# Optimization experiments

Hardware: AMD Instinct MI355X
Metric: run time of the kernel (lower is better)

## Reference

```python
import jax, jax.numpy as jnp
import numpy as np

N = 25600          # total nodes
B = 64             # graphs in batch
NPG = N // B       # nodes per graph (400)
K = 16             # in-degree (regular graph)
E = N * K          # edges
D = 128            # hidden dim = out dim
L = 4              # DGN layers
NUM_ATOM = 128


def _linear_init(key, out_s, in_s):
    lim = 1.0 / np.sqrt(in_s)
    return jax.random.uniform(key, (out_s, in_s), jnp.float32, -lim, lim)


def setup_inputs() -> dict:
    key = jax.random.key(0)
    ks = jax.random.split(key, 16)
    node_feat = jax.random.randint(ks[0], (N,), 0, NUM_ATOM)
    # K-regular in-degree graph, edges intra-graph; dst sorted
    dst = jnp.repeat(jnp.arange(N), K)                       # [E]
    src_local = jax.random.randint(ks[1], (E,), 0, NPG)
    src = (dst // NPG) * NPG + src_local                     # same graph as dst
    eig = jax.random.normal(ks[2], (E, 2), jnp.float32)
    snorm_n = jnp.full((N, 1), 1.0 / np.sqrt(NPG), jnp.float32)
    graph_ids = jnp.arange(N) // NPG
    emb = jax.random.normal(ks[3], (NUM_ATOM, D), jnp.float32) * 0.02
    pre_W = jnp.stack([_linear_init(jax.random.fold_in(ks[4], i), D, 2 * D) for i in range(L)])
    pre_b = jnp.zeros((L, D), jnp.float32)
    post_W = jnp.stack([_linear_init(jax.random.fold_in(ks[5], i), D, 5 * D) for i in range(L)])
    post_b = jnp.zeros((L, D), jnp.float32)
    r_W0 = _linear_init(ks[6], 64, 128); r_b0 = jnp.zeros((64,), jnp.float32)
    r_W1 = _linear_init(ks[7], 32, 64);  r_b1 = jnp.zeros((32,), jnp.float32)
    r_W2 = _linear_init(ks[8], 128, 32); r_b2 = jnp.zeros((128,), jnp.float32)
    return dict(node_feat=node_feat, src=src, dst=dst, eig=eig, snorm_n=snorm_n,
                graph_ids=graph_ids, emb=emb, pre_W=pre_W, pre_b=pre_b,
                post_W=post_W, post_b=post_b, r_W0=r_W0, r_b0=r_b0,
                r_W1=r_W1, r_b1=r_b1, r_W2=r_W2, r_b2=r_b2)


def _dgn_layer(h, src, dst, eig, snorm_n, Wp, bp, Wq, bq):
    n = h.shape[0]
    # pretrans on edges: Linear(cat(h_src, h_dst))  [E, D]
    z2 = jnp.concatenate([h[src], h[dst]], axis=-1)
    e = jnp.einsum('ei,oi->eo', z2, Wp) + bp
    seg_sum = lambda v: jax.ops.segment_sum(v, dst, num_segments=n, indices_are_sorted=True)
    s = seg_sum(e)
    mean = s / K
    mx = jax.ops.segment_max(e, dst, num_segments=n, indices_are_sorted=True)
    # directional aggregator (eig_idx=1)
    w = eig[:, 1]
    denom = seg_sum(jnp.abs(w)) + 1e-8                       # [n]
    ew = w / denom[dst]                                      # [E]
    dir_agg = jnp.abs(seg_sum(e * ew[:, None]) - seg_sum(ew)[:, None] * h)
    agg = jnp.concatenate([h, mean, s, mx, dir_agg], axis=-1)  # [n, 5D]
    hn = jnp.einsum('ni,oi->no', agg, Wq) + bq
    hn = hn * snorm_n           # graph_norm
    hn = jax.nn.relu(hn)
    return h + hn               # residual (in_dim == out_dim)


def reference(node_feat, src, dst, eig, snorm_n, graph_ids, emb,
              pre_W, pre_b, post_W, post_b,
              r_W0, r_b0, r_W1, r_b1, r_W2, r_b2):
    h = emb[node_feat]                                       # AtomEncoder
    for i in range(L):
        h = _dgn_layer(h, src, dst, eig, snorm_n, pre_W[i], pre_b[i], post_W[i], post_b[i])
    # mean_nodes per graph (equal-sized graphs)
    hg = jax.ops.segment_sum(h, graph_ids, num_segments=B, indices_are_sorted=True) / NPG
    y = jax.nn.relu(hg @ r_W0.T + r_b0)
    y = jax.nn.relu(y @ r_W1.T + r_b1)
    return y @ r_W2.T + r_b2                                 # [B, 128]
```

## Files before the change

kernel.cpp:

```cpp
#include <hip/hip_runtime.h>
#include <cstddef>

#define NN 25600
#define BB 64
#define NPG 400
#define KK 16
#define LL 4

typedef _Float16 half_t;
typedef _Float16 h8 __attribute__((ext_vector_type(8)));
typedef _Float16 h4 __attribute__((ext_vector_type(4)));
typedef _Float16 h2 __attribute__((ext_vector_type(2)));
typedef float f32x4 __attribute__((ext_vector_type(4)));

__global__ __launch_bounds__(256) void prep_k(const float* __restrict__ preW,
                                              const float* __restrict__ preb,
                                              const float* __restrict__ postW,
                                              half_t* __restrict__ WpreH,
                                              half_t* __restrict__ WpreL,
                                              float* __restrict__ bpre,
                                              half_t* __restrict__ WpostH,
                                              half_t* __restrict__ WpostL) {
  int idx = blockIdx.x * 256 + threadIdx.x;
  const int n1 = LL * 256 * 128;
  const int n2 = n1 + LL * 256;
  const int n3 = n2 + LL * 128 * 512;
  if (idx < n1) {
    int l = idx / 32768;
    int q = idx % 32768;
    int j = q & 7, lane = (q >> 3) & 63, kc = (q >> 9) & 3, c16 = q >> 11;
    int col = c16 * 16 + (lane & 15);
    int k = kc * 32 + (lane >> 4) * 8 + j;
    float v = (col < 128) ? preW[(size_t)l * 32768 + (size_t)col * 256 + k]
                          : preW[(size_t)l * 32768 + (size_t)(col - 128) * 256 + 128 + k];
    half_t hi = (half_t)v;
    WpreH[idx] = hi;
    WpreL[idx] = (half_t)(v - (float)hi);
  } else if (idx < n2) {
    int r = idx - n1;
    int l = r / 256, o = r % 256;
    bpre[r] = (o < 128) ? 0.f : preb[l * 128 + (o - 128)];
  } else if (idx < n3) {
    int r = idx - n2;
    int l = r / 65536;
    int q = r % 65536;
    int j = q & 7, lane = (q >> 3) & 63, kc = (q >> 9) & 15, c16 = q >> 13;
    int col = c16 * 16 + (lane & 15);
    int k = kc * 32 + (lane >> 4) * 8 + j;
    int jblk = k >> 7, kk = k & 127;
    const float* base = postW + (size_t)l * 128 * 640 + (size_t)col * 640;
    float v;
    if (jblk == 0)      v = base[kk];
    else if (jblk == 1) v = base[128 + kk] * (1.f / 16.f) + base[256 + kk];
    else if (jblk == 2) v = base[384 + kk];
    else                v = base[512 + kk];
    half_t hi = (half_t)v;
    WpostH[r] = hi;
    WpostL[r] = (half_t)(v - (float)hi);
  }
}

__global__ __launch_bounds__(256) void embed_k(const int* __restrict__ nf,
                                               const float* __restrict__ emb,
                                               half_t* __restrict__ Hh,
                                               half_t* __restrict__ Hl) {
  int idx = blockIdx.x * 256 + threadIdx.x;
  int n = idx >> 5;
  int d4 = idx & 31;
  int a = nf[n];
  float4 v = *(const float4*)(emb + (size_t)a * 128 + d4 * 4);
  h4 hi, lo;
  const float* vp = &v.x;
#pragma unroll
  for (int j = 0; j < 4; ++j) {
    half_t h = (half_t)vp[j];
    hi[j] = h;
    lo[j] = (half_t)(vp[j] - (float)h);
  }
  *(h4*)(Hh + (size_t)n * 128 + d4 * 4) = hi;
  *(h4*)(Hl + (size_t)n * 128 + d4 * 4) = lo;
}

__global__ __launch_bounds__(256) void pre_gemm_k(const half_t* __restrict__ Ah_g,
                                                  const half_t* __restrict__ Al_g,
                                                  const half_t* __restrict__ Wh_g,
                                                  const half_t* __restrict__ Wl_g,
                                                  float* __restrict__ preA) {
  __shared__ half_t Ahs[64][132];
  __shared__ half_t Als[64][132];
  const int tid = threadIdx.x;
  const int bid = blockIdx.x;
  const int swz = (bid & 7) * 50 + (bid >> 3);
  const int r0 = swz * 64;
  const int wid = tid >> 6, lane = tid & 63;
  const int wm = wid >> 1, wn = wid & 1;
  const int lr = lane & 15, lk = (lane >> 4) * 8;
  f32x4 acc[2][4] = {};

  {
    const int row = tid >> 2;
#pragma unroll
    for (int s = 0; s < 4; ++s) {
      const int koff = (tid & 3) * 8 + s * 32;
      const size_t g = (size_t)(r0 + row) * 128 + koff;
      *(h8*)&Ahs[row][koff] = *(const h8*)(Ah_g + g);
      *(h8*)&Als[row][koff] = *(const h8*)(Al_g + g);
    }
  }
  __syncthreads();

#pragma unroll
  for (int kc = 0; kc < 4; ++kc) {
    h8 af[2][2];
#pragma unroll
    for (int mi = 0; mi < 2; ++mi) {
      const int r = wm * 32 + mi * 16 + lr;
      af[mi][0] = *(const h8*)&Ahs[r][kc * 32 + lk];
      af[mi][1] = *(const h8*)&Als[r][kc * 32 + lk];
    }
#pragma unroll
    for (int nj = 0; nj < 4; ++nj) {
      const size_t fi = ((size_t)((wn * 4 + nj) * 4 + kc) * 64 + lane) * 8;
      const h8 b0v = *(const h8*)(Wh_g + fi);
      const h8 b1v = *(const h8*)(Wl_g + fi);
#pragma unroll
      for (int mi = 0; mi < 2; ++mi) {
        acc[mi][nj] = __builtin_amdgcn_mfma_f32_16x16x32_f16(af[mi][0], b0v, acc[mi][nj], 0, 0, 0);
        acc[mi][nj] = __builtin_amdgcn_mfma_f32_16x16x32_f16(af[mi][0], b1v, acc[mi][nj], 0, 0, 0);
        acc[mi][nj] = __builtin_amdgcn_mfma_f32_16x16x32_f16(af[mi][1], b0v, acc[mi][nj], 0, 0, 0);
      }
    }
  }
#pragma unroll
  for (int mi = 0; mi < 2; ++mi) {
    const int rowb = r0 + wm * 32 + mi * 16 + (lane >> 4) * 4;
#pragma unroll
    for (int nj = 0; nj < 4; ++nj) {
      const int col = wn * 64 + nj * 16 + lr;
#pragma unroll
      for (int q = 0; q < 4; ++q) {
        preA[(size_t)(rowb + q) * 128 + col] = acc[mi][nj][q];
      }
    }
  }
}

__global__ __launch_bounds__(256, 3) void agg_post_k(const float* __restrict__ preA,
                                                     const int* __restrict__ src,
                                                     const float* __restrict__ eig,
                                                     const half_t* __restrict__ WpHg,
                                                     const half_t* __restrict__ WpLg,
                                                     const float* __restrict__ bpre128,
                                                     half_t* __restrict__ Hh,
                                                     half_t* __restrict__ Hl,
                                                     const half_t* __restrict__ Wh,
                                                     const half_t* __restrict__ Wl,
                                                     const float* __restrict__ bias,
                                                     const float* __restrict__ snorm) {
  __shared__ half_t Ah[16][392];
  __shared__ half_t Al[16][392];
  __shared__ float bsh[16][132];
  const int tid = threadIdx.x;
  const int bid = blockIdx.x;
  const int swz = (bid & 7) * 200 + (bid >> 3);
  const int r0 = swz * 16;
  const int wid = tid >> 6, lane = tid & 63;
  const int wn = wid;
  const int lr = lane & 15, lk = (lane >> 4) * 8;
  const int gsel = lane >> 5;
  const int m4 = (lane & 31) * 4;

  const int frow = r0 + lr;
  h8 afh[4][2];
#pragma unroll
  for (int hc = 0; hc < 4; ++hc) {
    afh[hc][0] = *(const h8*)(Hh + (size_t)frow * 128 + hc * 32 + lk);
    afh[hc][1] = *(const h8*)(Hl + (size_t)frow * 128 + hc * 32 + lk);
  }

  {
    f32x4 bacc[2] = {};
#pragma unroll
    for (int kc = 0; kc < 4; ++kc) {
#pragma unroll
      for (int nj = 0; nj < 2; ++nj) {
        const size_t fi = ((size_t)((8 + wn * 2 + nj) * 4 + kc) * 64 + lane) * 8;
        const h8 b0v = *(const h8*)(WpHg + fi);
        const h8 b1v = *(const h8*)(WpLg + fi);
        bacc[nj] = __builtin_amdgcn_mfma_f32_16x16x32_f16(afh[kc][0], b0v, bacc[nj], 0, 0, 0);
        bacc[nj] = __builtin_amdgcn_mfma_f32_16x16x32_f16(afh[kc][0], b1v, bacc[nj], 0, 0, 0);
        bacc[nj] = __builtin_amdgcn_mfma_f32_16x16x32_f16(afh[kc][1], b0v, bacc[nj], 0, 0, 0);
      }
    }
    const int rowb = (lane >> 4) * 4;
#pragma unroll
    for (int nj = 0; nj < 2; ++nj) {
      const int col = (wn * 2 + nj) * 16 + lr;
      const float bv = bpre128[col];
#pragma unroll
      for (int q = 0; q < 4; ++q) {
        bsh[rowb + q][col] = bacc[nj][q] + bv;
      }
    }
  }
  __syncthreads();

#pragma unroll
  for (int i = 0; i < 4; ++i) {
    const int lrow = wid * 4 + i;
    const int n = r0 + lrow;
    int sv[KK];
    float wv[KK];
    {
      const int4* sp4 = (const int4*)(src + (size_t)n * KK);
      const float4* ep4 = (const float4*)(eig + (size_t)n * KK * 2);
#pragma unroll
      for (int t = 0; t < 4; ++t) {
        const int4 s4 = sp4[t];
        sv[4 * t + 0] = s4.x;
        sv[4 * t + 1] = s4.y;
        sv[4 * t + 2] = s4.z;
        sv[4 * t + 3] = s4.w;
      }
#pragma unroll
      for (int t = 0; t < 8; ++t) {
        const float4 e4 = ep4[t];
        wv[2 * t + 0] = e4.y;
        wv[2 * t + 1] = e4.w;
      }
    }
    float4 g0 = *(const float4*)(preA + (size_t)sv[0 + gsel] * 128 + m4);
    float4 g1 = *(const float4*)(preA + (size_t)sv[2 + gsel] * 128 + m4);
    float4 g2 = *(const float4*)(preA + (size_t)sv[4 + gsel] * 128 + m4);
    float4 g3 = *(const float4*)(preA + (size_t)sv[6 + gsel] * 128 + m4);
    float4 g4 = *(const float4*)(preA + (size_t)sv[8 + gsel] * 128 + m4);
    float4 g5 = *(const float4*)(preA + (size_t)sv[10 + gsel] * 128 + m4);
    float4 g6 = *(const float4*)(preA + (size_t)sv[12 + gsel] * 128 + m4);
    float4 g7 = *(const float4*)(preA + (size_t)sv[14 + gsel] * 128 + m4);
    float denom = 0.f;
#pragma unroll
    for (int e = 0; e < KK; ++e) denom += fabsf(wv[e]);
    denom += 1e-8f;
    const float inv = 1.f / denom;
    float sum_ew = 0.f;
#pragma unroll
    for (int e = 0; e < KK; ++e) {
      wv[e] *= inv;
      sum_ew += wv[e];
    }
    float sx = 0.f, sy = 0.f, sz = 0.f, sw_ = 0.f;
    float wx = 0.f, wy = 0.f, wz = 0.f, ww = 0.f;
    float mx = -3.402823466e+38f, my = mx, mz = mx, mw = mx;
#define ACC(G, J)                                                   \
    {                                                               \
      const float we = wv[2 * (J) + gsel];                          \
      sx += G.x; sy += G.y; sz += G.z; sw_ += G.w;                  \
      wx = fmaf(we, G.x, wx); wy = fmaf(we, G.y, wy);               \
      wz = fmaf(we, G.z, wz); ww = fmaf(we, G.w, ww);               \
      mx = fmaxf(mx, G.x); my = fmaxf(my, G.y);                     \
      mz = fmaxf(mz, G.z); mw = fmaxf(mw, G.w);                     \
    }
    ACC(g0, 0) ACC(g1, 1) ACC(g2, 2) ACC(g3, 3)
    ACC(g4, 4) ACC(g5, 5) ACC(g6, 6) ACC(g7, 7)
#undef ACC
    sx += __shfl_xor(sx, 32); sy += __shfl_xor(sy, 32);
    sz += __shfl_xor(sz, 32); sw_ += __shfl_xor(sw_, 32);
    wx += __shfl_xor(wx, 32); wy += __shfl_xor(wy, 32);
    wz += __shfl_xor(wz, 32); ww += __shfl_xor(ww, 32);
    mx = fmaxf(mx, __shfl_xor(mx, 32)); my = fmaxf(my, __shfl_xor(my, 32));
    mz = fmaxf(mz, __shfl_xor(mz, 32)); mw = fmaxf(mw, __shfl_xor(mw, 32));

    if (lane < 32) {
      const float4 b4 = *(const float4*)&bsh[lrow][m4];
      const h4 hh4 = *(const h4*)(Hh + (size_t)n * 128 + m4);
      const h4 hl4 = *(const h4*)(Hl + (size_t)n * 128 + m4);
      const float h0 = (float)hh4[0] + (float)hl4[0];
      const float h1 = (float)hh4[1] + (float)hl4[1];
      const float h2v = (float)hh4[2] + (float)hl4[2];
      const float h3 = (float)hh4[3] + (float)hl4[3];
      auto wr4 = [&](int kcol, float v0, float v1, float v2, float v3) {
        h4 hi, lo;
        hi[0] = (half_t)v0; lo[0] = (half_t)(v0 - (float)hi[0]);
        hi[1] = (half_t)v1; lo[1] = (half_t)(v1 - (float)hi[1]);
        hi[2] = (half_t)v2; lo[2] = (half_t)(v2 - (float)hi[2]);
        hi[3] = (half_t)v3; lo[3] = (half_t)(v3 - (float)hi[3]);
        *(h4*)&Ah[lrow][kcol] = hi;
        *(h4*)&Al[lrow][kcol] = lo;
      };
      wr4(m4, sx + 16.f * b4.x, sy + 16.f * b4.y, sz + 16.f * b4.z, sw_ + 16.f * b4.w);
      wr4(128 + m4, mx + b4.x, my + b4.y, mz + b4.z, mw + b4.w);
      wr4(256 + m4,
          fabsf(wx + sum_ew * (b4.x - h0)), fabsf(wy + sum_ew * (b4.y - h1)),
          fabsf(wz + sum_ew * (b4.z - h2v)), fabsf(ww + sum_ew * (b4.w - h3)));
    }
  }
  __syncthreads();

  f32x4 acc[2] = {};
#pragma unroll
  for (int kc = 0; kc < 16; ++kc) {
    h8 a0, a1;
    if (kc < 4) {
      a0 = afh[kc & 3][0];
      a1 = afh[kc & 3][1];
    } else {
      a0 = *(const h8*)&Ah[lr][(kc - 4) * 32 + lk];
      a1 = *(const h8*)&Al[lr][(kc - 4) * 32 + lk];
    }
#pragma unroll
    for (int nj = 0; nj < 2; ++nj) {
      const size_t fi = ((size_t)((wn * 2 + nj) * 16 + kc) * 64 + lane) * 8;
      const h8 b0v = *(const h8*)(Wh + fi);
      const h8 b1v = *(const h8*)(Wl + fi);
      acc[nj] = __builtin_amdgcn_mfma_f32_16x16x32_f16(a0, b0v, acc[nj], 0, 0, 0);
      acc[nj] = __builtin_amdgcn_mfma_f32_16x16x32_f16(a0, b1v, acc[nj], 0, 0, 0);
      acc[nj] = __builtin_amdgcn_mfma_f32_16x16x32_f16(a1, b0v, acc[nj], 0, 0, 0);
    }
  }

  const int rowb = r0 + (lane >> 4) * 4;
#pragma unroll
  for (int nj = 0; nj < 2; ++nj) {
    const int col = wn * 32 + nj * 16 + lr;
    const float bv = bias[col];
#pragma unroll
    for (int q = 0; q < 4; ++q) {
      const int r = rowb + q;
      float a = acc[nj][q] + bv;
      a *= snorm[r];
      a = fmaxf(a, 0.f);
      const size_t off = (size_t)r * 128 + col;
      const float hold = (float)Hh[off] + (float)Hl[off];
      const float hn = hold + a;
      const half_t hi = (half_t)hn;
      Hh[off] = hi;
      Hl[off] = (half_t)(hn - (float)hi);
    }
  }
}

__global__ __launch_bounds__(256) void reduce_mlp_k(const half_t* __restrict__ Hh,
                                                    const half_t* __restrict__ Hl,
                                                    const float* __restrict__ W0, const float* __restrict__ b0,
                                                    const float* __restrict__ W1, const float* __restrict__ b1,
                                                    const float* __restrict__ W2, const float* __restrict__ b2,
                                                    float* __restrict__ out) {
  __shared__ float hgs[128];
  __shared__ float red[128];
  __shared__ float y0s[64];
  __shared__ float y1s[32];
  __shared__ float wb[64 * 130];
  const int g = blockIdx.x;
  const int t = threadIdx.x;
  {
    const int d = t & 127, hf = t >> 7;
    const size_t base = ((size_t)g * NPG + (size_t)hf * 200) * 128 + d;
    float acc = 0.f;
    for (int i = 0; i < 200; ++i) {
      const size_t off = base + (size_t)i * 128;
      acc += (float)Hh[off] + (float)Hl[off];
    }
    if (hf) red[d] = acc;
    __syncthreads();
    if (!hf) hgs[d] = (acc + red[d]) * (1.f / (float)NPG);
  }
  __syncthreads();
  for (int idx = t; idx < 64 * 128; idx += 256) {
    wb[(idx >> 7) * 130 + (idx & 127)] = W0[idx];
  }
  __syncthreads();
  if (t < 64) {
    float a = b0[t];
    const float* w = &wb[t * 130];
    for (int k = 0; k < 128; ++k) a = fmaf(hgs[k], w[k], a);
    y0s[t] = fmaxf(a, 0.f);
  }
  __syncthreads();
  for (int idx = t; idx < 32 * 64; idx += 256) {
    wb[(idx >> 6) * 66 + (idx & 63)] = W1[idx];
  }
  __syncthreads();
  if (t < 32) {
    float a = b1[t];
    const float* w = &wb[t * 66];
    for (int k = 0; k < 64; ++k) a = fmaf(y0s[k], w[k], a);
    y1s[t] = fmaxf(a, 0.f);
  }
  __syncthreads();
  for (int idx = t; idx < 128 * 32; idx += 256) {
    wb[(idx >> 5) * 34 + (idx & 31)] = W2[idx];
  }
  __syncthreads();
  if (t < 128) {
    float a = b2[t];
    const float* w = &wb[t * 34];
    for (int k = 0; k < 32; ++k) a = fmaf(y1s[k], w[k], a);
    out[(size_t)g * 128 + t] = a;
  }
}

extern "C" void kernel_launch(void* const* d_in, const int* in_sizes, int n_in,
                              void* d_out, int out_size, void* d_ws, size_t ws_size,
                              hipStream_t stream) {
  const int* node_feat = (const int*)d_in[0];
  const int* src = (const int*)d_in[1];
  const float* eig = (const float*)d_in[3];
  const float* snorm = (const float*)d_in[4];
  const float* emb = (const float*)d_in[6];
  const float* preW = (const float*)d_in[7];
  const float* preb = (const float*)d_in[8];
  const float* postW = (const float*)d_in[9];
  const float* postb = (const float*)d_in[10];
  const float* rW0 = (const float*)d_in[11];
  const float* rb0 = (const float*)d_in[12];
  const float* rW1 = (const float*)d_in[13];
  const float* rb1 = (const float*)d_in[14];
  const float* rW2 = (const float*)d_in[15];
  const float* rb2 = (const float*)d_in[16];
  float* out = (float*)d_out;

  half_t* Hh = (half_t*)d_ws;
  half_t* Hl = Hh + (size_t)NN * 128;
  float* preA = (float*)(Hl + (size_t)NN * 128);
  half_t* WpreH = (half_t*)(preA + (size_t)NN * 128);
  half_t* WpreL = WpreH + (size_t)LL * 32768;
  half_t* WpostH = WpreL + (size_t)LL * 32768;
  half_t* WpostL = WpostH + (size_t)LL * 65536;
  float* bpre = (float*)(WpostL + (size_t)LL * 65536);

  prep_k<<<1540, 256, 0, stream>>>(preW, preb, postW, WpreH, WpreL, bpre, WpostH, WpostL);
  embed_k<<<(NN * 32) / 256, 256, 0, stream>>>(node_feat, emb, Hh, Hl);

  for (int l = 0; l < LL; ++l) {
    pre_gemm_k<<<NN / 64, 256, 0, stream>>>(
        Hh, Hl, WpreH + (size_t)l * 32768, WpreL + (size_t)l * 32768, preA);
    agg_post_k<<<NN / 16, 256, 0, stream>>>(
        preA, src, eig,
        WpreH + (size_t)l * 32768, WpreL + (size_t)l * 32768,
        bpre + (size_t)l * 256 + 128,
        Hh, Hl,
        WpostH + (size_t)l * 65536, WpostL + (size_t)l * 65536,
        postb + (size_t)l * 128, snorm);
  }

  reduce_mlp_k<<<BB, 256, 0, stream>>>(Hh, Hl, rW0, rb0, rW1, rb1, rW2, rb2, out);
}
```

Measured before the change: 267.1 us.

## Split fused aggregate+post-GEMM into separate agg and post-GEMM kernels

The dst-half of the pre-transform GEMM moves into pre_gemm_k as a second grid dimension, which writes a per-node bias buffer. The former fused agg_post_k is split into agg_k, with one wave per node writing the full 512-wide split-fp16 aggregate row to global memory, and post_gemm_k, which loads those rows into LDS and runs the MFMA GEMM. This is meant to raise occupancy and parallelism of the gather phase and remove redundant per-block work. The cost is extra global round trips of the aggregate matrix (hi and lo, 512 halves per node) and one more launch per layer.

```diff
diff --git a/kernel.cpp b/kernel.cpp
--- a/kernel.cpp
+++ b/kernel.cpp
@@ -85,11 +85,14 @@
                                                   const half_t* __restrict__ Al_g,
                                                   const half_t* __restrict__ Wh_g,
                                                   const half_t* __restrict__ Wl_g,
-                                                  float* __restrict__ preA) {
+                                                  const float* __restrict__ bpre128,
+                                                  float* __restrict__ preA,
+                                                  float* __restrict__ bF) {
   __shared__ half_t Ahs[64][132];
   __shared__ half_t Als[64][132];
   const int tid = threadIdx.x;
   const int bid = blockIdx.x;
+  const int y = blockIdx.y;
   const int swz = (bid & 7) * 50 + (bid >> 3);
   const int r0 = swz * 64;
   const int wid = tid >> 6, lane = tid & 63;
@@ -120,7 +123,7 @@
     }
 #pragma unroll
     for (int nj = 0; nj < 4; ++nj) {
-      const size_t fi = ((size_t)((wn * 4 + nj) * 4 + kc) * 64 + lane) * 8;
+      const size_t fi = ((size_t)((y * 8 + wn * 4 + nj) * 4 + kc) * 64 + lane) * 8;
       const h8 b0v = *(const h8*)(Wh_g + fi);
       const h8 b1v = *(const h8*)(Wl_g + fi);
 #pragma unroll
@@ -131,35 +134,134 @@
       }
     }
   }
+  float* outp = (y == 0) ? preA : bF;
 #pragma unroll
   for (int mi = 0; mi < 2; ++mi) {
     const int rowb = r0 + wm * 32 + mi * 16 + (lane >> 4) * 4;
 #pragma unroll
     for (int nj = 0; nj < 4; ++nj) {
       const int col = wn * 64 + nj * 16 + lr;
+      const float bv = (y == 0) ? 0.f : bpre128[col];
 #pragma unroll
       for (int q = 0; q < 4; ++q) {
-        preA[(size_t)(rowb + q) * 128 + col] = acc[mi][nj][q];
+        outp[(size_t)(rowb + q) * 128 + col] = acc[mi][nj][q] + bv;
       }
     }
   }
 }
 
-__global__ __launch_bounds__(256, 3) void agg_post_k(const float* __restrict__ preA,
-                                                     const int* __restrict__ src,
-                                                     const float* __restrict__ eig,
-                                                     const half_t* __restrict__ WpHg,
-                                                     const half_t* __restrict__ WpLg,
-                                                     const float* __restrict__ bpre128,
-                                                     half_t* __restrict__ Hh,
-                                                     half_t* __restrict__ Hl,
-                                                     const half_t* __restrict__ Wh,
-                                                     const half_t* __restrict__ Wl,
-                                                     const float* __restrict__ bias,
-                                                     const float* __restrict__ snorm) {
-  __shared__ half_t Ah[16][392];
-  __shared__ half_t Al[16][392];
-  __shared__ float bsh[16][132];
+__global__ __launch_bounds__(256) void agg_k(const float* __restrict__ preA,
+                                             const float* __restrict__ bF,
+                                             const int* __restrict__ src,
+                                             const float* __restrict__ eig,
+                                             const half_t* __restrict__ Hh,
+                                             const half_t* __restrict__ Hl,
+                                             half_t* __restrict__ AhG,
+                                             half_t* __restrict__ AlG) {
+  const int bid = blockIdx.x;
+  const int swz = (bid & 7) * 800 + (bid >> 3);
+  const int wid = threadIdx.x >> 6, lane = threadIdx.x & 63;
+  const int n = swz * 4 + wid;
+  const int gsel = lane >> 5;
+  const int m4 = (lane & 31) * 4;
+
+  int sv[KK];
+  float wv[KK];
+  {
+    const int4* sp4 = (const int4*)(src + (size_t)n * KK);
+    const float4* ep4 = (const float4*)(eig + (size_t)n * KK * 2);
+#pragma unroll
+    for (int t = 0; t < 4; ++t) {
+      const int4 s4 = sp4[t];
+      sv[4 * t + 0] = s4.x; sv[4 * t + 1] = s4.y;
+      sv[4 * t + 2] = s4.z; sv[4 * t + 3] = s4.w;
+    }
+#pragma unroll
+    for (int t = 0; t < 8; ++t) {
+      const float4 e4 = ep4[t];
+      wv[2 * t + 0] = e4.y; wv[2 * t + 1] = e4.w;
+    }
+  }
+  float4 g0 = *(const float4*)(preA + (size_t)sv[0 + gsel] * 128 + m4);
+  float4 g1 = *(const float4*)(preA + (size_t)sv[2 + gsel] * 128 + m4);
+  float4 g2 = *(const float4*)(preA + (size_t)sv[4 + gsel] * 128 + m4);
+  float4 g3 = *(const float4*)(preA + (size_t)sv[6 + gsel] * 128 + m4);
+  float4 g4 = *(const float4*)(preA + (size_t)sv[8 + gsel] * 128 + m4);
+  float4 g5 = *(const float4*)(preA + (size_t)sv[10 + gsel] * 128 + m4);
+  float4 g6 = *(const float4*)(preA + (size_t)sv[12 + gsel] * 128 + m4);
+  float4 g7 = *(const float4*)(preA + (size_t)sv[14 + gsel] * 128 + m4);
+  float denom = 0.f;
+#pragma unroll
+  for (int e = 0; e < KK; ++e) denom += fabsf(wv[e]);
+  denom += 1e-8f;
+  const float inv = 1.f / denom;
+  float sum_ew = 0.f;
+#pragma unroll
+  for (int e = 0; e < KK; ++e) {
+    wv[e] *= inv;
+    sum_ew += wv[e];
+  }
+  float sx = 0.f, sy = 0.f, sz = 0.f, sw_ = 0.f;
+  float wx = 0.f, wy = 0.f, wz = 0.f, ww = 0.f;
+  float mx = -3.402823466e+38f, my = mx, mz = mx, mw = mx;
+#define ACC(G, J)                                                   \
+  {                                                                 \
+    const float we = wv[2 * (J) + gsel];                            \
+    sx += G.x; sy += G.y; sz += G.z; sw_ += G.w;                    \
+    wx = fmaf(we, G.x, wx); wy = fmaf(we, G.y, wy);                 \
+    wz = fmaf(we, G.z, wz); ww = fmaf(we, G.w, ww);                 \
+    mx = fmaxf(mx, G.x); my = fmaxf(my, G.y);                       \
+    mz = fmaxf(mz, G.z); mw = fmaxf(mw, G.w);                       \
+  }
+  ACC(g0, 0) ACC(g1, 1) ACC(g2, 2) ACC(g3, 3)
+  ACC(g4, 4) ACC(g5, 5) ACC(g6, 6) ACC(g7, 7)
+#undef ACC
+  sx += __shfl_xor(sx, 32); sy += __shfl_xor(sy, 32);
+  sz += __shfl_xor(sz, 32); sw_ += __shfl_xor(sw_, 32);
+  wx += __shfl_xor(wx, 32); wy += __shfl_xor(wy, 32);
+  wz += __shfl_xor(wz, 32); ww += __shfl_xor(ww, 32);
+  mx = fmaxf(mx, __shfl_xor(mx, 32)); my = fmaxf(my, __shfl_xor(my, 32));
+  mz = fmaxf(mz, __shfl_xor(mz, 32)); mw = fmaxf(mw, __shfl_xor(mw, 32));
+
+  if (lane < 32) {
+    const float4 b4 = *(const float4*)(bF + (size_t)n * 128 + m4);
+    const h4 hh4 = *(const h4*)(Hh + (size_t)n * 128 + m4);
+    const h4 hl4 = *(const h4*)(Hl + (size_t)n * 128 + m4);
+    const float h0 = (float)hh4[0] + (float)hl4[0];
+    const float h1 = (float)hh4[1] + (float)hl4[1];
+    const float h2v = (float)hh4[2] + (float)hl4[2];
+    const float h3 = (float)hh4[3] + (float)hl4[3];
+    half_t* ah = AhG + (size_t)n * 512;
+    half_t* al = AlG + (size_t)n * 512;
+    *(h4*)(ah + m4) = hh4;
+    *(h4*)(al + m4) = hl4;
+    auto wr4 = [&](int kcol, float v0, float v1, float v2, float v3) {
+      h4 hi, lo;
+      hi[0] = (half_t)v0; lo[0] = (half_t)(v0 - (float)hi[0]);
+      hi[1] = (half_t)v1; lo[1] = (half_t)(v1 - (float)hi[1]);
+      hi[2] = (half_t)v2; lo[2] = (half_t)(v2 - (float)hi[2]);
+      hi[3] = (half_t)v3; lo[3] = (half_t)(v3 - (float)hi[3]);
+      *(h4*)(ah + kcol) = hi;
+      *(h4*)(al + kcol) = lo;
+    };
+    wr4(128 + m4, sx + 16.f * b4.x, sy + 16.f * b4.y, sz + 16.f * b4.z, sw_ + 16.f * b4.w);
+    wr4(256 + m4, mx + b4.x, my + b4.y, mz + b4.z, mw + b4.w);
+    wr4(384 + m4,
+        fabsf(wx + sum_ew * (b4.x - h0)), fabsf(wy + sum_ew * (b4.y - h1)),
+        fabsf(wz + sum_ew * (b4.z - h2v)), fabsf(ww + sum_ew * (b4.w - h3)));
+  }
+}
+
+__global__ __launch_bounds__(256) void post_gemm_k(const half_t* __restrict__ AhG,
+                                                   const half_t* __restrict__ AlG,
+                                                   const half_t* __restrict__ Wh,
+                                                   const half_t* __restrict__ Wl,
+                                                   const float* __restrict__ bias,
+                                                   const float* __restrict__ snorm,
+                                                   half_t* __restrict__ Hh,
+                                                   half_t* __restrict__ Hl) {
+  __shared__ half_t AhS[16][520];
+  __shared__ half_t AlS[16][520];
   const int tid = threadIdx.x;
   const int bid = blockIdx.x;
   const int swz = (bid & 7) * 200 + (bid >> 3);
@@ -167,146 +269,22 @@
   const int wid = tid >> 6, lane = tid & 63;
   const int wn = wid;
   const int lr = lane & 15, lk = (lane >> 4) * 8;
-  const int gsel = lane >> 5;
-  const int m4 = (lane & 31) * 4;
-
-  const int frow = r0 + lr;
-  h8 afh[4][2];
-#pragma unroll
-  for (int hc = 0; hc < 4; ++hc) {
-    afh[hc][0] = *(const h8*)(Hh + (size_t)frow * 128 + hc * 32 + lk);
-    afh[hc][1] = *(const h8*)(Hl + (size_t)frow * 128 + hc * 32 + lk);
-  }
-
-  {
-    f32x4 bacc[2] = {};
-#pragma unroll
-    for (int kc = 0; kc < 4; ++kc) {
-#pragma unroll
-      for (int nj = 0; nj < 2; ++nj) {
-        const size_t fi = ((size_t)((8 + wn * 2 + nj) * 4 + kc) * 64 + lane) * 8;
-        const h8 b0v = *(const h8*)(WpHg + fi);
-        const h8 b1v = *(const h8*)(WpLg + fi);
-        bacc[nj] = __builtin_amdgcn_mfma_f32_16x16x32_f16(afh[kc][0], b0v, bacc[nj], 0, 0, 0);
-        bacc[nj] = __builtin_amdgcn_mfma_f32_16x16x32_f16(afh[kc][0], b1v, bacc[nj], 0, 0, 0);
-        bacc[nj] = __builtin_amdgcn_mfma_f32_16x16x32_f16(afh[kc][1], b0v, bacc[nj], 0, 0, 0);
-      }
-    }
-    const int rowb = (lane >> 4) * 4;
-#pragma unroll
-    for (int nj = 0; nj < 2; ++nj) {
-      const int col = (wn * 2 + nj) * 16 + lr;
-      const float bv = bpre128[col];
-#pragma unroll
-      for (int q = 0; q < 4; ++q) {
-        bsh[rowb + q][col] = bacc[nj][q] + bv;
-      }
-    }
-  }
-  __syncthreads();
-
-#pragma unroll
-  for (int i = 0; i < 4; ++i) {
-    const int lrow = wid * 4 + i;
-    const int n = r0 + lrow;
-    int sv[KK];
-    float wv[KK];
-    {
-      const int4* sp4 = (const int4*)(src + (size_t)n * KK);
-      const float4* ep4 = (const float4*)(eig + (size_t)n * KK * 2);
-#pragma unroll
-      for (int t = 0; t < 4; ++t) {
-        const int4 s4 = sp4[t];
-        sv[4 * t + 0] = s4.x;
-        sv[4 * t + 1] = s4.y;
-        sv[4 * t + 2] = s4.z;
-        sv[4 * t + 3] = s4.w;
-      }
-#pragma unroll
-      for (int t = 0; t < 8; ++t) {
-        const float4 e4 = ep4[t];
-        wv[2 * t + 0] = e4.y;
-        wv[2 * t + 1] = e4.w;
-      }
-    }
-    float4 g0 = *(const float4*)(preA + (size_t)sv[0 + gsel] * 128 + m4);
-    float4 g1 = *(const float4*)(preA + (size_t)sv[2 + gsel] * 128 + m4);
-    float4 g2 = *(const float4*)(preA + (size_t)sv[4 + gsel] * 128 + m4);
-    float4 g3 = *(const float4*)(preA + (size_t)sv[6 + gsel] * 128 + m4);
-    float4 g4 = *(const float4*)(preA + (size_t)sv[8 + gsel] * 128 + m4);
-    float4 g5 = *(const float4*)(preA + (size_t)sv[10 + gsel] * 128 + m4);
-    float4 g6 = *(const float4*)(preA + (size_t)sv[12 + gsel] * 128 + m4);
-    float4 g7 = *(const float4*)(preA + (size_t)sv[14 + gsel] * 128 + m4);
-    float denom = 0.f;
-#pragma unroll
-    for (int e = 0; e < KK; ++e) denom += fabsf(wv[e]);
-    denom += 1e-8f;
-    const float inv = 1.f / denom;
-    float sum_ew = 0.f;
-#pragma unroll
-    for (int e = 0; e < KK; ++e) {
-      wv[e] *= inv;
-      sum_ew += wv[e];
-    }
-    float sx = 0.f, sy = 0.f, sz = 0.f, sw_ = 0.f;
-    float wx = 0.f, wy = 0.f, wz = 0.f, ww = 0.f;
-    float mx = -3.402823466e+38f, my = mx, mz = mx, mw = mx;
-#define ACC(G, J)                                                   \
-    {                                                               \
-      const float we = wv[2 * (J) + gsel];                          \
-      sx += G.x; sy += G.y; sz += G.z; sw_ += G.w;                  \
-      wx = fmaf(we, G.x, wx); wy = fmaf(we, G.y, wy);               \
-      wz = fmaf(we, G.z, wz); ww = fmaf(we, G.w, ww);               \
-      mx = fmaxf(mx, G.x); my = fmaxf(my, G.y);                     \
-      mz = fmaxf(mz, G.z); mw = fmaxf(mw, G.w);                     \
-    }
-    ACC(g0, 0) ACC(g1, 1) ACC(g2, 2) ACC(g3, 3)
-    ACC(g4, 4) ACC(g5, 5) ACC(g6, 6) ACC(g7, 7)
-#undef ACC
-    sx += __shfl_xor(sx, 32); sy += __shfl_xor(sy, 32);
-    sz += __shfl_xor(sz, 32); sw_ += __shfl_xor(sw_, 32);
-    wx += __shfl_xor(wx, 32); wy += __shfl_xor(wy, 32);
-    wz += __shfl_xor(wz, 32); ww += __shfl_xor(ww, 32);
-    mx = fmaxf(mx, __shfl_xor(mx, 32)); my = fmaxf(my, __shfl_xor(my, 32));
-    mz = fmaxf(mz, __shfl_xor(mz, 32)); mw = fmaxf(mw, __shfl_xor(mw, 32));
-
-    if (lane < 32) {
-      const float4 b4 = *(const float4*)&bsh[lrow][m4];
-      const h4 hh4 = *(const h4*)(Hh + (size_t)n * 128 + m4);
-      const h4 hl4 = *(const h4*)(Hl + (size_t)n * 128 + m4);
-      const float h0 = (float)hh4[0] + (float)hl4[0];
-      const float h1 = (float)hh4[1] + (float)hl4[1];
-      const float h2v = (float)hh4[2] + (float)hl4[2];
-      const float h3 = (float)hh4[3] + (float)hl4[3];
-      auto wr4 = [&](int kcol, float v0, float v1, float v2, float v3) {
-        h4 hi, lo;
-        hi[0] = (half_t)v0; lo[0] = (half_t)(v0 - (float)hi[0]);
-        hi[1] = (half_t)v1; lo[1] = (half_t)(v1 - (float)hi[1]);
-        hi[2] = (half_t)v2; lo[2] = (half_t)(v2 - (float)hi[2]);
-        hi[3] = (half_t)v3; lo[3] = (half_t)(v3 - (float)hi[3]);
-        *(h4*)&Ah[lrow][kcol] = hi;
-        *(h4*)&Al[lrow][kcol] = lo;
-      };
-      wr4(m4, sx + 16.f * b4.x, sy + 16.f * b4.y, sz + 16.f * b4.z, sw_ + 16.f * b4.w);
-      wr4(128 + m4, mx + b4.x, my + b4.y, mz + b4.z, mw + b4.w);
-      wr4(256 + m4,
-          fabsf(wx + sum_ew * (b4.x - h0)), fabsf(wy + sum_ew * (b4.y - h1)),
-          fabsf(wz + sum_ew * (b4.z - h2v)), fabsf(ww + sum_ew * (b4.w - h3)));
-    }
+
+#pragma unroll
+  for (int it = 0; it < 4; ++it) {
+    const int id = it * 256 + tid;
+    const int r = id >> 6;
+    const int c = (id & 63) * 8;
+    *(h8*)&AhS[r][c] = *(const h8*)(AhG + (size_t)(r0 + r) * 512 + c);
+    *(h8*)&AlS[r][c] = *(const h8*)(AlG + (size_t)(r0 + r) * 512 + c);
   }
   __syncthreads();
 
   f32x4 acc[2] = {};
 #pragma unroll
   for (int kc = 0; kc < 16; ++kc) {
-    h8 a0, a1;
-    if (kc < 4) {
-      a0 = afh[kc & 3][0];
-      a1 = afh[kc & 3][1];
-    } else {
-      a0 = *(const h8*)&Ah[lr][(kc - 4) * 32 + lk];
-      a1 = *(const h8*)&Al[lr][(kc - 4) * 32 + lk];
-    }
+    const h8 a0 = *(const h8*)&AhS[lr][kc * 32 + lk];
+    const h8 a1 = *(const h8*)&AlS[lr][kc * 32 + lk];
 #pragma unroll
     for (int nj = 0; nj < 2; ++nj) {
       const size_t fi = ((size_t)((wn * 2 + nj) * 16 + kc) * 64 + lane) * 8;
@@ -318,7 +296,7 @@
     }
   }
 
-  const int rowb = r0 + (lane >> 4) * 4;
+  const int rowb = (lane >> 4) * 4;
 #pragma unroll
   for (int nj = 0; nj < 2; ++nj) {
     const int col = wn * 32 + nj * 16 + lr;
@@ -326,13 +304,14 @@
 #pragma unroll
     for (int q = 0; q < 4; ++q) {
       const int r = rowb + q;
+      const int grow = r0 + r;
       float a = acc[nj][q] + bv;
-      a *= snorm[r];
+      a *= snorm[grow];
       a = fmaxf(a, 0.f);
-      const size_t off = (size_t)r * 128 + col;
-      const float hold = (float)Hh[off] + (float)Hl[off];
+      const float hold = (float)AhS[r][col] + (float)AlS[r][col];
       const float hn = hold + a;
       const half_t hi = (half_t)hn;
+      const size_t off = (size_t)grow * 128 + col;
       Hh[off] = hi;
       Hl[off] = (half_t)(hn - (float)hi);
     }
@@ -422,7 +401,10 @@
   half_t* Hh = (half_t*)d_ws;
   half_t* Hl = Hh + (size_t)NN * 128;
   float* preA = (float*)(Hl + (size_t)NN * 128);
-  half_t* WpreH = (half_t*)(preA + (size_t)NN * 128);
+  float* bF = preA + (size_t)NN * 128;
+  half_t* AhG = (half_t*)(bF + (size_t)NN * 128);
+  half_t* AlG = AhG + (size_t)NN * 512;
+  half_t* WpreH = AlG + (size_t)NN * 512;
   half_t* WpreL = WpreH + (size_t)LL * 32768;
   half_t* WpostH = WpreL + (size_t)LL * 32768;
   half_t* WpostL = WpostH + (size_t)LL * 65536;
@@ -432,15 +414,13 @@
   embed_k<<<(NN * 32) / 256, 256, 0, stream>>>(node_feat, emb, Hh, Hl);
 
   for (int l = 0; l < LL; ++l) {
-    pre_gemm_k<<<NN / 64, 256, 0, stream>>>(
-        Hh, Hl, WpreH + (size_t)l * 32768, WpreL + (size_t)l * 32768, preA);
-    agg_post_k<<<NN / 16, 256, 0, stream>>>(
-        preA, src, eig,
-        WpreH + (size_t)l * 32768, WpreL + (size_t)l * 32768,
-        bpre + (size_t)l * 256 + 128,
-        Hh, Hl,
-        WpostH + (size_t)l * 65536, WpostL + (size_t)l * 65536,
-        postb + (size_t)l * 128, snorm);
+    pre_gemm_k<<<dim3(NN / 64, 2), 256, 0, stream>>>(
+        Hh, Hl, WpreH + (size_t)l * 32768, WpreL + (size_t)l * 32768,
+        bpre + (size_t)l * 256 + 128, preA, bF);
+    agg_k<<<NN / 4, 256, 0, stream>>>(preA, bF, src, eig, Hh, Hl, AhG, AlG);
+    post_gemm_k<<<NN / 16, 256, 0, stream>>>(
+        AhG, AlG, WpostH + (size_t)l * 65536, WpostL + (size_t)l * 65536,
+        postb + (size_t)l * 128, snorm, Hh, Hl);
   }
 
   reduce_mlp_k<<<BB, 256, 0, stream>>>(Hh, Hl, rW0, rb0, rW1, rb1, rW2, rb2, out);
```

Result: slower. 324.1 us (+21.4%).
